# Performance work log

Hardware: AMD Instinct MI355X
Metric: run time of the kernel (lower is better)

## Reference

```python
import math
import jax, jax.numpy as jnp
import numpy as np

B, T, HIDDEN = 2, 2048, 1024
H, HKV, D = 16, 16, 64


def _rope_tables(T, D):
    inv_freq = 1.0 / (10000.0 ** (jnp.arange(0, D, 2, dtype=jnp.float32) / D))
    t = jnp.arange(T, dtype=jnp.float32)
    freqs = jnp.outer(t, inv_freq)               # [T, D/2]
    emb = jnp.concatenate([freqs, freqs], axis=-1)  # [T, D]
    return jnp.cos(emb), jnp.sin(emb)


def setup_inputs() -> dict:
    key = jax.random.key(0)
    k1, k2, k3 = jax.random.split(key, 3)
    hidden_states = jax.random.normal(k1, (B, T, HIDDEN), dtype=jnp.float32)
    cos, sin = _rope_tables(T, D)
    # trunc-normal-ish init, std = 1/sqrt(fan_in)
    w_qkv = jax.random.normal(k2, ((H + 2 * HKV) * D, HIDDEN), dtype=jnp.float32) / math.sqrt(HIDDEN)
    w_o = jax.random.normal(k3, (HIDDEN, H * D), dtype=jnp.float32) / math.sqrt(H * D)
    return {"hidden_states": hidden_states, "cos": cos, "sin": sin, "w_qkv": w_qkv, "w_o": w_o}


def _rotate_half(x):
    x1, x2 = jnp.split(x, 2, axis=-1)
    return jnp.concatenate([-x2, x1], axis=-1)


def reference(hidden_states, cos, sin, w_qkv, w_o):
    b, t, _ = hidden_states.shape
    # fused QKV projection: [B,T,(H+2*HKV)*D]
    qkv = jnp.einsum('bti,oi->bto', hidden_states, w_qkv)
    qkv = qkv.reshape(b, t, H + 2 * HKV, D)
    q = qkv[:, :, :H]                    # [B,T,H,D]
    k = qkv[:, :, H:H + HKV]             # [B,T,HKV,D]
    v = qkv[:, :, H + HKV:]              # [B,T,HKV,D]
    # inline RoPE; cos/sin broadcast over heads
    c = cos[:, None, :]
    s = sin[:, None, :]
    q = q * c + _rotate_half(q) * s
    k = k * c + _rotate_half(k) * s
    scale = 1.0 / math.sqrt(D)
    attn_scores = jnp.einsum('bthd,bThd->bhtT', q, k) * scale  # [B,H,T,T]
    mask = jnp.tril(jnp.ones((t, t), dtype=bool))
    attn_scores = jnp.where(mask[None, None, :, :], attn_scores, -1e9)
    attn = jax.nn.softmax(attn_scores, axis=-1)
    context = jnp.einsum('bhtT,bThd->bthd', attn, v).reshape(b, t, H * D)
    return jnp.einsum('bti,oi->bto', context, w_o)
```

## Files before the change

### kernel.cpp

```cpp
#include <hip/hip_runtime.h>

typedef __bf16 bf16_t;
typedef __bf16 bf16x4 __attribute__((ext_vector_type(4)));
typedef __bf16 bf16x8 __attribute__((ext_vector_type(8)));
typedef float f32x4 __attribute__((ext_vector_type(4)));
typedef unsigned long long u64;

#define MFMA16(a, b, c) __builtin_amdgcn_mfma_f32_16x16x32_bf16((a), (b), (c), 0, 0, 0)

__device__ inline bf16x8 load8(const float* p) {
    const f32x4 a = *(const f32x4*)p;
    const f32x4 b = *(const f32x4*)(p + 4);
    bf16x8 r;
#pragma unroll
    for (int i = 0; i < 4; i++) { r[i] = (bf16_t)a[i]; r[4 + i] = (bf16_t)b[i]; }
    return r;
}
__device__ inline bf16x8 load8(const bf16_t* p) { return *(const bf16x8*)p; }

__device__ inline bf16x4 shfl4(bf16x4 v, int src) {
    u64 x;
    __builtin_memcpy(&x, &v, 8);
    x = __shfl(x, src, 64);
    bf16x4 r;
    __builtin_memcpy(&r, &x, 8);
    return r;
}


template <int MODE, int NDIM, int BM, typename TA>
__global__ __launch_bounds__(256) void gemm_bt(const TA* __restrict__ A,
                                               const float* __restrict__ B,
                                               float* __restrict__ outp,
                                               bf16_t* __restrict__ q_ws,
                                               bf16_t* __restrict__ k_ws,
                                               bf16_t* __restrict__ v_ws,
                                               const float* __restrict__ cosb,
                                               const float* __restrict__ sinb) {
    constexpr int K = 1024;
    constexpr int IM = BM / 32;
    __shared__ __align__(16) bf16_t As[BM * 32];
    __shared__ __align__(16) bf16_t Bs[128 * 32];

    const int tid = threadIdx.x;
    const int w = tid >> 6;
    const int lane = tid & 63;
    const int lr = lane & 15;
    const int quad = lane >> 4;
    const int m0 = blockIdx.y * BM;
    const int n0 = blockIdx.x * 128;
    const int wm = (w & 1) * (BM / 2);
    const int wn = (w >> 1) * 64;

    const int srow = tid >> 2;
    const int skk = (tid & 3) * 8;
    const TA* gA0 = A + (size_t)(m0 + srow) * K + skk;
    const TA* gA1 = gA0 + (size_t)64 * K;
    const float* gB0 = B + (size_t)(n0 + srow) * K + skk;
    const float* gB1 = gB0 + (size_t)64 * K;

    f32x4 acc[IM][4] = {};

    for (int k0 = 0; k0 < K; k0 += 32) {
        const bf16x8 ra0 = load8(gA0 + k0);
        bf16x8 ra1;
        if constexpr (BM == 128) ra1 = load8(gA1 + k0);
        const bf16x8 rb0 = load8(gB0 + k0);
        const bf16x8 rb1 = load8(gB1 + k0);
        __syncthreads();
        *(bf16x8*)&As[srow * 32 + skk] = ra0;
        if constexpr (BM == 128) *(bf16x8*)&As[(64 + srow) * 32 + skk] = ra1;
        *(bf16x8*)&Bs[srow * 32 + skk] = rb0;
        *(bf16x8*)&Bs[(64 + srow) * 32 + skk] = rb1;
        __syncthreads();

        bf16x8 af[IM], bfm[4];
#pragma unroll
        for (int im = 0; im < IM; im++)
            af[im] = *(const bf16x8*)&As[(wm + im * 16 + lr) * 32 + quad * 8];
#pragma unroll
        for (int in = 0; in < 4; in++)
            bfm[in] = *(const bf16x8*)&Bs[(wn + in * 16 + lr) * 32 + quad * 8];
#pragma unroll
        for (int im = 0; im < IM; im++)
#pragma unroll
            for (int in = 0; in < 4; in++)
                acc[im][in] = MFMA16(af[im], bfm[in], acc[im][in]);
    }

    if constexpr (MODE == 0) {
#pragma unroll
        for (int im = 0; im < IM; im++)
#pragma unroll
            for (int in = 0; in < 4; in++)
#pragma unroll
                for (int r = 0; r < 4; r++) {
                    const int m = m0 + wm + im * 16 + quad * 4 + r;
                    const int n = n0 + wn + in * 16 + lr;
                    outp[(size_t)m * NDIM + n] = acc[im][in][r];
                }
    } else {
        const int j = (n0 + wn) >> 6;
        if (j < 32) {
            const bool isq = (j < 16);
            const float qs = 0.125f * 1.44269504089f;
#pragma unroll
            for (int im = 0; im < IM; im++) {
#pragma unroll
                for (int r = 0; r < 4; r++) {
                    const int m = m0 + wm + im * 16 + quad * 4 + r;
                    const int b = m >> 11;
                    const int t = m & 2047;
#pragma unroll
                    for (int in = 0; in < 2; in++) {
                        const int d = in * 16 + lr;
                        const float x1 = acc[im][in][r];
                        const float x2 = acc[im][in + 2][r];
                        const float c = cosb[t * 64 + d];
                        const float s = sinb[t * 64 + d];
                        float y1 = x1 * c - x2 * s;
                        float y2 = x2 * c + x1 * s;
                        if (isq) {
                            y1 *= qs; y2 *= qs;
                            const size_t base =
                                ((size_t)(b * 16 + j) * 2048 + t) * 64 + d;
                            q_ws[base] = (bf16_t)y1;
                            q_ws[base + 32] = (bf16_t)y2;
                        } else {
                            const int bh = b * 16 + (j - 16);
                            const size_t off =
                                ((size_t)(bh * 128 + (t >> 4)) * 2) * 512 +
                                ((t & 15) + (d >> 3) * 16) * 8 + (d & 7);
                            k_ws[off] = (bf16_t)y1;
                            k_ws[off + 512] = (bf16_t)y2;
                        }
                    }
                }
            }
        } else {
#pragma unroll
            for (int im = 0; im < IM; im++)
#pragma unroll
                for (int in = 0; in < 4; in++)
#pragma unroll
                    for (int r = 0; r < 4; r++) {
                        const int m = m0 + wm + im * 16 + quad * 4 + r;
                        const int b = m >> 11;
                        const int t = m & 2047;
                        const int d = in * 16 + lr;
                        const int bh = b * 16 + (j - 32);
                        const size_t off =
                            ((size_t)(bh * 64 + (t >> 5)) * 4 + (d >> 4)) * 512 +
                            ((d & 15) + ((t & 31) >> 3) * 16) * 8 + (t & 7);
                        v_ws[off] = (bf16_t)acc[im][in][r];
                    }
        }
    }
}

__global__ __launch_bounds__(256) void attn_kernel(const bf16_t* __restrict__ q_ws,
                                                   const bf16_t* __restrict__ k_ws,
                                                   const bf16_t* __restrict__ v_ws,
                                                   bf16_t* __restrict__ ctx) {
    const int tid = threadIdx.x;
    const int w = tid >> 6;
    const int lane = tid & 63;
    const int lr = lane & 15;
    const int quad = lane >> 4;
    const int bh = blockIdx.x & 31;
    const int qt = 31 - (blockIdx.x >> 5);
    const int trow = qt * 64 + w * 16;
    const int query = trow + lr;

    const bf16_t* qb = q_ws + ((size_t)bh * 2048 + trow + lr) * 64 + quad * 8;
    const bf16x8 qlo = *(const bf16x8*)qb;
    const bf16x8 qhi = *(const bf16x8*)(qb + 32);

    const bf16_t* kbase = k_ws + (size_t)bh * 131072 + lane * 8;
    const bf16_t* vbase = v_ws + (size_t)bh * 131072 + lane * 8;

    f32x4 o[4] = {};
    float lrun = 0.0f;

    const int srcLow = ((quad & 1) << 5) + lr;
    const int srcHigh = srcLow + 16;
    const bool loSel = (quad < 2);

    bf16x8 kc[8];
#pragma unroll
    for (int n = 0; n < 4; n++) {
        kc[2 * n] = *(const bf16x8*)(kbase + (size_t)(n * 2) * 512);
        kc[2 * n + 1] = *(const bf16x8*)(kbase + (size_t)(n * 2 + 1) * 512);
    }

    for (int kb = 0; kb <= qt; kb++) {
        bf16x8 vv[2][4];
#pragma unroll
        for (int hh = 0; hh < 2; hh++)
#pragma unroll
            for (int n = 0; n < 4; n++)
                vv[hh][n] = *(const bf16x8*)(vbase +
                    (size_t)((kb * 2 + hh) * 4 + n) * 512);

        const int kbn = (kb < qt) ? kb + 1 : kb;
        bf16x8 kn[8];
#pragma unroll
        for (int n = 0; n < 4; n++) {
            kn[2 * n] = *(const bf16x8*)(kbase + (size_t)((kbn * 4 + n) * 2) * 512);
            kn[2 * n + 1] = *(const bf16x8*)(kbase + (size_t)((kbn * 4 + n) * 2 + 1) * 512);
        }

        const int u0 = kb * 64;
        f32x4 s[4];
#pragma unroll
        for (int n = 0; n < 4; n++) {
            const f32x4 z = {};
            s[n] = MFMA16(kc[2 * n], qlo, z);
            s[n] = MFMA16(kc[2 * n + 1], qhi, s[n]);
        }

        if (kb == qt) {
#pragma unroll
            for (int n = 0; n < 4; n++)
#pragma unroll
                for (int r = 0; r < 4; r++)
                    if (u0 + n * 16 + quad * 4 + r > query) s[n][r] = -1e9f;
        }

        f32x4 p[4];
#pragma unroll
        for (int n = 0; n < 4; n++)
#pragma unroll
            for (int r = 0; r < 4; r++) p[n][r] = exp2f(s[n][r]);

        lrun += ((p[0][0] + p[0][1]) + (p[0][2] + p[0][3])) +
                ((p[1][0] + p[1][1]) + (p[1][2] + p[1][3])) +
                ((p[2][0] + p[2][1]) + (p[2][2] + p[2][3])) +
                ((p[3][0] + p[3][1]) + (p[3][2] + p[3][3]));

        bf16x4 pb[4];
#pragma unroll
        for (int n = 0; n < 4; n++)
#pragma unroll
            for (int r = 0; r < 4; r++) pb[n][r] = (bf16_t)p[n][r];

#pragma unroll
        for (int hh = 0; hh < 2; hh++) {
            const bf16x4 a0 = shfl4(pb[2 * hh], srcLow);
            const bf16x4 a1 = shfl4(pb[2 * hh + 1], srcLow);
            const bf16x4 b0 = shfl4(pb[2 * hh], srcHigh);
            const bf16x4 b1 = shfl4(pb[2 * hh + 1], srcHigh);
            const bf16x4 lo = loSel ? a0 : a1;
            const bf16x4 hi = loSel ? b0 : b1;
            bf16x8 pf;
#pragma unroll
            for (int r = 0; r < 4; r++) { pf[r] = lo[r]; pf[4 + r] = hi[r]; }

#pragma unroll
            for (int n = 0; n < 4; n++)
                o[n] = MFMA16(vv[hh][n], pf, o[n]);
        }

#pragma unroll
        for (int i = 0; i < 8; i++) kc[i] = kn[i];
    }

    lrun += __shfl_xor(lrun, 16);
    lrun += __shfl_xor(lrun, 32);

    const int b = bh >> 4;
    const int hd = bh & 15;
    const float inv = 1.0f / fmaxf(lrun, 1e-30f);
    const size_t base = ((size_t)b * 2048 + query) * 1024 + hd * 64 + quad * 4;
#pragma unroll
    for (int n = 0; n < 4; n++) {
        bf16x4 ob;
#pragma unroll
        for (int r = 0; r < 4; r++) ob[r] = (bf16_t)(o[n][r] * inv);
        *(bf16x4*)&ctx[base + n * 16] = ob;
    }
}

extern "C" void kernel_launch(void* const* d_in, const int* in_sizes, int n_in,
                              void* d_out, int out_size, void* d_ws, size_t ws_size,
                              hipStream_t stream) {
    const float* hs = (const float*)d_in[0];
    const float* cosb = (const float*)d_in[1];
    const float* sinb = (const float*)d_in[2];
    const float* wqkv = (const float*)d_in[3];
    const float* wo = (const float*)d_in[4];
    float* out = (float*)d_out;

    char* ws = (char*)d_ws;
    bf16_t* q_ws = (bf16_t*)(ws);
    bf16_t* k_ws = (bf16_t*)(ws + (size_t)(8u << 20));
    bf16_t* v_ws = (bf16_t*)(ws + (size_t)(16u << 20));
    bf16_t* ctx = (bf16_t*)(ws + (size_t)(24u << 20));

    const dim3 blk(256);

    gemm_bt<1, 3072, 128><<<dim3(24, 32), blk, 0, stream>>>(
        hs, wqkv, nullptr, q_ws, k_ws, v_ws, cosb, sinb);

    attn_kernel<<<dim3(1024), blk, 0, stream>>>(q_ws, k_ws, v_ws, ctx);

    gemm_bt<0, 1024, 64><<<dim3(8, 64), blk, 0, stream>>>(
        ctx, wo, out, nullptr, nullptr, nullptr, nullptr, nullptr);
}
```

Measured before the change: 200.2 us.

## Pre-convert inputs to bf16 and stage GEMM tiles with direct global-to-LDS loads

Adds a conversion kernel that turns the hidden states and both weight matrices into bf16 in the workspace, so both GEMMs read half-width operands instead of converting fp32 on every tile load. The GEMM tile loads now use global_load_lds to write straight into shared memory without going through registers, with a second barrier added at the end of each k-step. The workspace is rearranged so the attention context reuses the converted hidden-state region. The trade is an extra launch plus a full read/write pass over about 10M elements, in exchange for less GEMM load traffic and fewer register-staged conversions.

```diff
diff --git a/kernel.cpp b/kernel.cpp
--- a/kernel.cpp
+++ b/kernel.cpp
@@ -8,6 +8,11 @@
 
 #define MFMA16(a, b, c) __builtin_amdgcn_mfma_f32_16x16x32_bf16((a), (b), (c), 0, 0, 0)
 
+#define LDG2LDS16(g, l)                                                        \
+    __builtin_amdgcn_global_load_lds(                                          \
+        (const __attribute__((address_space(1))) void*)(g),                    \
+        (__attribute__((address_space(3))) void*)(l), 16, 0, 0)
+
 __device__ inline bf16x8 load8(const float* p) {
     const f32x4 a = *(const f32x4*)p;
     const f32x4 b = *(const f32x4*)(p + 4);
@@ -16,7 +21,6 @@
     for (int i = 0; i < 4; i++) { r[i] = (bf16_t)a[i]; r[4 + i] = (bf16_t)b[i]; }
     return r;
 }
-__device__ inline bf16x8 load8(const bf16_t* p) { return *(const bf16x8*)p; }
 
 __device__ inline bf16x4 shfl4(bf16x4 v, int src) {
     u64 x;
@@ -27,10 +31,23 @@
     return r;
 }
 
-
-template <int MODE, int NDIM, int BM, typename TA>
-__global__ __launch_bounds__(256) void gemm_bt(const TA* __restrict__ A,
-                                               const float* __restrict__ B,
+__global__ __launch_bounds__(256) void convert_kernel(const float* __restrict__ hs,
+                                                      const float* __restrict__ wqkv,
+                                                      const float* __restrict__ wo,
+                                                      bf16_t* __restrict__ outb) {
+    const size_t c = ((size_t)blockIdx.x * 256 + threadIdx.x) * 8;
+    const float* src;
+    size_t off;
+    if (c < 4194304) { src = hs; off = c; }
+    else if (c < 7340032) { src = wqkv; off = c - 4194304; }
+    else { src = wo; off = c - 7340032; }
+    *(bf16x8*)(outb + c) = load8(src + off);
+}
+
+
+template <int MODE, int NDIM, int BM>
+__global__ __launch_bounds__(256) void gemm_bt(const bf16_t* __restrict__ A,
+                                               const bf16_t* __restrict__ B,
                                                float* __restrict__ outp,
                                                bf16_t* __restrict__ q_ws,
                                                bf16_t* __restrict__ k_ws,
@@ -54,24 +71,22 @@
 
     const int srow = tid >> 2;
     const int skk = (tid & 3) * 8;
-    const TA* gA0 = A + (size_t)(m0 + srow) * K + skk;
-    const TA* gA1 = gA0 + (size_t)64 * K;
-    const float* gB0 = B + (size_t)(n0 + srow) * K + skk;
-    const float* gB1 = gB0 + (size_t)64 * K;
+    const bf16_t* gA0 = A + (size_t)(m0 + srow) * K + skk;
+    const bf16_t* gA1 = gA0 + (size_t)64 * K;
+    const bf16_t* gB0 = B + (size_t)(n0 + srow) * K + skk;
+    const bf16_t* gB1 = gB0 + (size_t)64 * K;
+    bf16_t* lA0 = As + w * 512;
+    bf16_t* lA1 = As + 2048 + w * 512;
+    bf16_t* lB0 = Bs + w * 512;
+    bf16_t* lB1 = Bs + 2048 + w * 512;
 
     f32x4 acc[IM][4] = {};
 
     for (int k0 = 0; k0 < K; k0 += 32) {
-        const bf16x8 ra0 = load8(gA0 + k0);
-        bf16x8 ra1;
-        if constexpr (BM == 128) ra1 = load8(gA1 + k0);
-        const bf16x8 rb0 = load8(gB0 + k0);
-        const bf16x8 rb1 = load8(gB1 + k0);
-        __syncthreads();
-        *(bf16x8*)&As[srow * 32 + skk] = ra0;
-        if constexpr (BM == 128) *(bf16x8*)&As[(64 + srow) * 32 + skk] = ra1;
-        *(bf16x8*)&Bs[srow * 32 + skk] = rb0;
-        *(bf16x8*)&Bs[(64 + srow) * 32 + skk] = rb1;
+        LDG2LDS16(gA0 + k0, lA0);
+        if constexpr (BM == 128) LDG2LDS16(gA1 + k0, lA1);
+        LDG2LDS16(gB0 + k0, lB0);
+        LDG2LDS16(gB1 + k0, lB1);
         __syncthreads();
 
         bf16x8 af[IM], bfm[4];
@@ -86,6 +101,7 @@
 #pragma unroll
             for (int in = 0; in < 4; in++)
                 acc[im][in] = MFMA16(af[im], bfm[in], acc[im][in]);
+        __syncthreads();
     }
 
     if constexpr (MODE == 0) {
@@ -292,18 +308,23 @@
     float* out = (float*)d_out;
 
     char* ws = (char*)d_ws;
-    bf16_t* q_ws = (bf16_t*)(ws);
-    bf16_t* k_ws = (bf16_t*)(ws + (size_t)(8u << 20));
-    bf16_t* v_ws = (bf16_t*)(ws + (size_t)(16u << 20));
-    bf16_t* ctx = (bf16_t*)(ws + (size_t)(24u << 20));
+    bf16_t* hs_b = (bf16_t*)(ws);
+    bf16_t* wqkv_b = hs_b + 4194304;
+    bf16_t* wo_b = hs_b + 7340032;
+    bf16_t* q_ws = (bf16_t*)(ws + (size_t)(16u << 20));
+    bf16_t* k_ws = (bf16_t*)(ws + (size_t)(24u << 20));
+    bf16_t* v_ws = (bf16_t*)(ws + (size_t)(32u << 20));
+    bf16_t* ctx = (bf16_t*)(ws);
 
     const dim3 blk(256);
 
+    convert_kernel<<<dim3(4096), blk, 0, stream>>>(hs, wqkv, wo, hs_b);
+
     gemm_bt<1, 3072, 128><<<dim3(24, 32), blk, 0, stream>>>(
-        hs, wqkv, nullptr, q_ws, k_ws, v_ws, cosb, sinb);
+        hs_b, wqkv_b, nullptr, q_ws, k_ws, v_ws, cosb, sinb);
 
     attn_kernel<<<dim3(1024), blk, 0, stream>>>(q_ws, k_ws, v_ws, ctx);
 
     gemm_bt<0, 1024, 64><<<dim3(8, 64), blk, 0, stream>>>(
-        ctx, wo, out, nullptr, nullptr, nullptr, nullptr, nullptr);
-}
+        ctx, wo_b, out, nullptr, nullptr, nullptr, nullptr, nullptr);
+}
```

New measurement: 181.1 us. 1.11x faster.
